# Optimization experiments

Measured on AMD Instinct MI355X. Metric: run time of the kernel, lower is better.

Reference implementation:

```python
import jax, jax.numpy as jnp
import numpy as np

B, N, NPOINT, NSAMPLE = 16, 4096, 1024, 32
RADIUS = 0.2
CHANNELS = [6, 64, 64, 128]
EPS = 1e-5


def farthest_point_sample(xyz, npoint):
    # xyz: [B,N,3] -> idx [B,npoint]; deterministic start at index 0
    b, n, _ = xyz.shape
    def step(carry, _):
        dist, far = carry
        centroid = jnp.take_along_axis(xyz, far[:, None, None], axis=1)  # [B,1,3]
        d = jnp.sum((xyz - centroid) ** 2, axis=-1)  # [B,N]
        dist = jnp.minimum(dist, d)
        return (dist, jnp.argmax(dist, axis=-1).astype(jnp.int32)), far
    init = (jnp.full((b, n), 1e10, dtype=xyz.dtype), jnp.zeros((b,), jnp.int32))
    _, cents = jax.lax.scan(step, init, None, length=npoint)
    return cents.T  # [B,npoint]


def query_ball_point(radius, nsample, xyz, new_xyz):
    # xyz [B,N,3], new_xyz [B,S,3] -> idx [B,S,nsample]
    b, n, _ = xyz.shape
    d2 = (jnp.sum(new_xyz ** 2, -1)[:, :, None]
          + jnp.sum(xyz ** 2, -1)[:, None, :]
          - 2.0 * jnp.einsum('bsc,bnc->bsn', new_xyz, xyz))  # [B,S,N]
    cand = jnp.where(d2 > radius * radius, n, jnp.arange(n, dtype=jnp.int32)[None, None, :])
    # smallest nsample candidate indices (== torch sort[:, :, :nsample])
    neg_top, _ = jax.lax.top_k(-cand, nsample)
    idx = -neg_top  # ascending smallest indices
    first = idx[:, :, 0:1]
    return jnp.where(idx == n, first, idx)


def gather_points(pts, idx):
    # pts [B,N,C], idx [B,S,K] -> [B,S,K,C]
    b, s, k = idx.shape
    flat = idx.reshape(b, s * k)
    out = jnp.take_along_axis(pts, flat[:, :, None], axis=1)
    return out.reshape(b, s, k, pts.shape[-1])


def _forward(xyz, points, params):
    fps_idx = farthest_point_sample(xyz, NPOINT)  # [B,S]
    new_xyz = jnp.take_along_axis(xyz, fps_idx[:, :, None], axis=1)  # [B,S,3]
    idx = query_ball_point(RADIUS, NSAMPLE, xyz, new_xyz)  # [B,S,K]
    grouped_xyz = gather_points(xyz, idx) - new_xyz[:, :, None, :]  # [B,S,K,3]
    grouped_pts = gather_points(points, idx)  # [B,S,K,D]
    x = jnp.concatenate([grouped_xyz, grouped_pts], axis=-1)  # [B,S,K,6]
    for (W, g, bta, m, v) in params:
        x = jnp.einsum('bskc,cd->bskd', x, W)
        x = (x - m) * (g * jax.lax.rsqrt(v + EPS)) + bta  # BN (inference stats)
        x = jax.nn.relu(x)
    feat = jnp.max(x, axis=2)  # [B,S,Cout]
    return new_xyz, feat


def setup_inputs() -> dict:
    key = jax.random.key(0)
    ks = jax.random.split(key, 16)
    xyz = jax.random.uniform(ks[0], (B, N, 3), dtype=jnp.float32)
    points = jax.random.normal(ks[1], (B, N, 3), dtype=jnp.float32)
    inp = {'xyz': xyz, 'points': points}
    ki = 2
    for li in range(3):
        cin, cout = CHANNELS[li], CHANNELS[li + 1]
        inp[f'W{li+1}'] = jax.random.normal(ks[ki], (cin, cout), dtype=jnp.float32) * (1.0 / np.sqrt(cin)); ki += 1
        inp[f'g{li+1}'] = jnp.ones((cout,), jnp.float32)
        inp[f'b{li+1}'] = jnp.zeros((cout,), jnp.float32)
        inp[f'm{li+1}'] = jax.random.normal(ks[ki], (cout,), dtype=jnp.float32) * 0.1; ki += 1
        inp[f'v{li+1}'] = jax.random.uniform(ks[ki], (cout,), dtype=jnp.float32, minval=0.5, maxval=1.5); ki += 1
    return inp


def reference(xyz, points, W1, g1, b1, m1, v1, W2, g2, b2, m2, v2, W3, g3, b3, m3, v3):
    params = [(W1, g1, b1, m1, v1), (W2, g2, b2, m2, v2), (W3, g3, b3, m3, v3)]
    return _forward(xyz, points, params)
```

## Files before the change

### kernel.cpp

```cpp
#include <hip/hip_runtime.h>

#define BATCH   16
#define NPTS    4096
#define NPOINT  1024
#define NSAMPLE 32

typedef float v2f __attribute__((ext_vector_type(2)));
typedef float v4f __attribute__((ext_vector_type(4)));
typedef const __attribute__((address_space(4))) float cs_float;
typedef const __attribute__((address_space(4))) v4f   cs_v4f;

__global__ __attribute__((amdgpu_waves_per_eu(1, 1))) __launch_bounds__(256)
void fps_kernel(const float* __restrict__ xyz, float* __restrict__ new_xyz)
{
#pragma clang fp contract(off)
    const int b    = blockIdx.x;
    const int t    = threadIdx.x;
    const int lane = t & 63;
    const int wv   = t >> 6;
    const float* xb = xyz + (size_t)b * NPTS * 3;

    __shared__ float sxyz4[NPTS * 4];
    __shared__ __align__(16) unsigned long long sCand[2][4];

    v2f px2[8], py2[8], pz2[8], dist2[8];
#pragma unroll
    for (int j = 0; j < 16; ++j) {
        const int n = j * 256 + t;
        float X = xb[n * 3 + 0];
        float Y = xb[n * 3 + 1];
        float Z = xb[n * 3 + 2];
        sxyz4[n * 4 + 0] = X; sxyz4[n * 4 + 1] = Y; sxyz4[n * 4 + 2] = Z;
        asm volatile("" : "+v"(X), "+v"(Y), "+v"(Z));
        const int p = j >> 1;
        if (j & 1) { px2[p].y = X; py2[p].y = Y; pz2[p].y = Z; dist2[p].y = 1e10f; }
        else       { px2[p].x = X; py2[p].x = Y; pz2[p].x = Z; dist2[p].x = 1e10f; }
    }
    __syncthreads();

    float cx = sxyz4[0], cy = sxyz4[1], cz = sxyz4[2];
    float* out = new_xyz + (size_t)b * NPOINT * 3;

    for (int i = 0; i < NPOINT; ++i) {
        if (t == 0) { out[i*3+0] = cx; out[i*3+1] = cy; out[i*3+2] = cz; }

        v2f c2x; c2x.x = cx; c2x.y = cx;
        v2f c2y; c2y.x = cy; c2y.y = cy;
        v2f c2z; c2z.x = cz; c2z.y = cz;
#pragma unroll
        for (int p = 0; p < 8; ++p) {
            v2f dx = px2[p] - c2x;
            v2f dy = py2[p] - c2y;
            v2f dz = pz2[p] - c2z;
            v2f xx = dx * dx;
            v2f yy = dy * dy;
            v2f zz = dz * dz;
            v2f ss = (xx + yy) + zz;
            dist2[p].x = fminf(dist2[p].x, ss.x);
            dist2[p].y = fminf(dist2[p].y, ss.y);
        }

#define D(j) ((j) & 1 ? dist2[(j) >> 1].y : dist2[(j) >> 1].x)
        float mA = fmaxf(fmaxf(D(0),  D(1)),  D(2));
        float mB = fmaxf(fmaxf(D(3),  D(4)),  D(5));
        float mC = fmaxf(fmaxf(D(6),  D(7)),  D(8));
        float mD = fmaxf(fmaxf(D(9),  D(10)), D(11));
        float mE = fmaxf(fmaxf(D(12), D(13)), D(14));
        float mx = fmaxf(fmaxf(fmaxf(mA, mB), mC),
                         fmaxf(fmaxf(mD, mE), D(15)));
        int bj = 15;
#pragma unroll
        for (int j = 15; j >= 0; --j) bj = (D(j) == mx) ? j : bj;
#undef D
        const int bidx = bj * 256 + t;

        unsigned long long cand =
            ((unsigned long long)__float_as_uint(mx) << 32) |
            (unsigned long long)(unsigned int)~bidx;

#define DPP_RED(CTRL, RMASK)                                                   \
        {                                                                      \
            unsigned int oh = (unsigned int)__builtin_amdgcn_update_dpp(       \
                0, (int)(unsigned int)(cand >> 32), (CTRL), (RMASK), 0xF, true);\
            unsigned int ol = (unsigned int)__builtin_amdgcn_update_dpp(       \
                0, (int)(unsigned int)cand, (CTRL), (RMASK), 0xF, true);       \
            unsigned long long o =                                             \
                ((unsigned long long)oh << 32) | (unsigned long long)ol;       \
            if (o > cand) cand = o;                                            \
        }
        DPP_RED(0x121, 0xF)
        DPP_RED(0x122, 0xF)
        DPP_RED(0x124, 0xF)
        DPP_RED(0x128, 0xF)
        DPP_RED(0x142, 0xA)
        DPP_RED(0x143, 0xC)
#undef DPP_RED

        const int par = i & 1;
        if (lane == 63) sCand[par][wv] = cand;
        asm volatile("s_waitcnt lgkmcnt(0)\n\ts_barrier" ::: "memory");

        const ulonglong2* pc = (const ulonglong2*)&sCand[par][0];
        ulonglong2 r0 = pc[0], r1 = pc[1];
        const float4* sx4 = (const float4*)sxyz4;
        float4 f0 = sx4[~(unsigned int)r0.x];
        float4 f1 = sx4[~(unsigned int)r0.y];
        float4 f2 = sx4[~(unsigned int)r1.x];
        float4 f3 = sx4[~(unsigned int)r1.y];
        bool s01 = r0.y > r0.x;
        bool s23 = r1.y > r1.x;
        unsigned long long m01 = s01 ? r0.y : r0.x;
        unsigned long long m23 = s23 ? r1.y : r1.x;
        float4 g01; g01.x = s01 ? f1.x : f0.x; g01.y = s01 ? f1.y : f0.y; g01.z = s01 ? f1.z : f0.z;
        float4 g23; g23.x = s23 ? f3.x : f2.x; g23.y = s23 ? f3.y : f2.y; g23.z = s23 ? f3.z : f2.z;
        bool sF = m23 > m01;
        cx = sF ? g23.x : g01.x;
        cy = sF ? g23.y : g01.y;
        cz = sF ? g23.z : g01.z;
    }
}

__global__ __launch_bounds__(256)
void ball_kernel(const float* __restrict__ xyz, const float* __restrict__ new_xyz,
                 int* __restrict__ idx)
{
    const int q    = blockIdx.x * 4 + (threadIdx.x >> 6);
    const int lane = threadIdx.x & 63;
    const int b    = q >> 10;
    const float* xb = xyz + (size_t)b * NPTS * 3;
    const int NCH = NPTS / 64;

    const float s0 = new_xyz[q*3+0];
    const float s1 = new_xyz[q*3+1];
    const float s2 = new_xyz[q*3+2];
    const float ssum = __fadd_rn(__fadd_rn(__fmul_rn(s0,s0), __fmul_rn(s1,s1)),
                                 __fmul_rn(s2,s2));
    const float r2 = (float)(0.2 * 0.2);

    int* myidx = idx + (size_t)q * NSAMPLE;
    int found = 0;
    int first = -1;

    float x = xb[lane*3+0], y = xb[lane*3+1], z = xb[lane*3+2];
    int c = 0;
    while (true) {
        float xn = 0.f, yn = 0.f, zn = 0.f;
        if (c + 1 < NCH) {
            const float* p = xb + ((size_t)(c + 1) * 64 + lane) * 3;
            xn = p[0]; yn = p[1]; zn = p[2];
        }

        int n = c * 64 + lane;
        float nsum = __fadd_rn(__fadd_rn(__fmul_rn(x,x), __fmul_rn(y,y)), __fmul_rn(z,z));
        float dot  = __fmaf_rn(s2, z, __fmaf_rn(s1, y, __fmul_rn(s0, x)));
        float d2   = __fsub_rn(__fadd_rn(ssum, nsum), __fmul_rn(2.0f, dot));
        bool inb = !(d2 > r2);
        unsigned long long m = __ballot(inb);
        if (first < 0 && m != 0ull) first = c * 64 + (int)__builtin_ctzll(m);
        if (inb) {
            int rank = __popcll(m & ((1ull << lane) - 1ull));
            int slot = found + rank;
            if (slot < NSAMPLE) myidx[slot] = n;
        }
        found += __popcll(m);

        ++c;
        if (c >= NCH || found >= NSAMPLE) break;
        x = xn; y = yn; z = zn;
    }
    if (found > NSAMPLE) found = NSAMPLE;
    for (int slot = found + lane; slot < NSAMPLE; slot += 64) myidx[slot] = first;
}

__global__ __launch_bounds__(256)
void prep_kernel(const float* __restrict__ W1, const float* __restrict__ g1,
                 const float* __restrict__ b1, const float* __restrict__ m1,
                 const float* __restrict__ v1,
                 const float* __restrict__ W2, const float* __restrict__ g2,
                 const float* __restrict__ b2, const float* __restrict__ m2,
                 const float* __restrict__ v2,
                 const float* __restrict__ W3, const float* __restrict__ g3,
                 const float* __restrict__ b3, const float* __restrict__ m3,
                 const float* __restrict__ v3,
                 float* __restrict__ wt)
{
    const int t = threadIdx.x;
    float* Wt1 = wt;
    float* Wt2 = wt + 512;
    float* Wt3 = wt + 512 + 4096;
    float* bi1 = wt + 512 + 4096 + 8192;
    float* bi2 = bi1 + 64;
    float* bi3 = bi2 + 64;

    for (int e = t; e < 64 * 8; e += 256) {
        int d = e >> 3, c = e & 7;
        float sc = g1[d] / sqrtf(v1[d] + 1e-5f);
        Wt1[e] = (c < 6) ? W1[c * 64 + d] * sc : 0.f;
    }
    for (int e = t; e < 64 * 64; e += 256) {
        int d = e >> 6, c = e & 63;
        float sc = g2[d] / sqrtf(v2[d] + 1e-5f);
        Wt2[e] = W2[c * 64 + d] * sc;
    }
    for (int e = t; e < 128 * 64; e += 256) {
        int d = e >> 6, c = e & 63;
        float sc = g3[d] / sqrtf(v3[d] + 1e-5f);
        Wt3[e] = W3[c * 128 + d] * sc;
    }
    for (int d = t; d < 64; d += 256) {
        float s1v = g1[d] / sqrtf(v1[d] + 1e-5f);
        bi1[d] = b1[d] - m1[d] * s1v;
        float s2v = g2[d] / sqrtf(v2[d] + 1e-5f);
        bi2[d] = b2[d] - m2[d] * s2v;
    }
    for (int d = t; d < 128; d += 256) {
        float s3v = g3[d] / sqrtf(v3[d] + 1e-5f);
        bi3[d] = b3[d] - m3[d] * s3v;
    }
}

__global__ __launch_bounds__(256)
void mlp_kernel(const float* __restrict__ xyz, const float* __restrict__ points,
                const float* __restrict__ new_xyz, const int* __restrict__ idx,
                const float* __restrict__ wt,
                float* __restrict__ feat)
{
    const cs_v4f*   Wc1 = (const cs_v4f*)(wt);
    const cs_v4f*   Wc2 = (const cs_v4f*)(wt + 512);
    const cs_v4f*   Wc3 = (const cs_v4f*)(wt + 512 + 4096);
    const cs_float* bi1 = (const cs_float*)(wt + 512 + 4096 + 8192);
    const cs_float* bi2 = bi1 + 64;
    const cs_float* bi3 = bi2 + 64;

    const int tid  = threadIdx.x;
    const int wid  = tid >> 6;
    const int lane = tid & 63;
    const int q = blockIdx.x * 8 + wid * 2 + (lane >> 5);
    const int k = lane & 31;
    const int b = q >> 10;

    const int n = idx[(size_t)q * NSAMPLE + k];
    const float* xp = xyz    + ((size_t)b * NPTS + n) * 3;
    const float* pp = points + ((size_t)b * NPTS + n) * 3;
    const float* nx = new_xyz + (size_t)q * 3;

    const float in0 = __fsub_rn(xp[0], nx[0]);
    const float in1 = __fsub_rn(xp[1], nx[1]);
    const float in2 = __fsub_rn(xp[2], nx[2]);
    const float in3 = pp[0], in4 = pp[1], in5 = pp[2];

    v2f x2[32];
#pragma unroll
    for (int d = 0; d < 64; ++d) {
        v4f wa = Wc1[d * 2 + 0];
        v4f wb = Wc1[d * 2 + 1];
        float acc = bi1[d];
        acc = fmaf(in0, wa.x, acc);
        acc = fmaf(in1, wa.y, acc);
        acc = fmaf(in2, wa.z, acc);
        acc = fmaf(in3, wa.w, acc);
        acc = fmaf(in4, wb.x, acc);
        acc = fmaf(in5, wb.y, acc);
        float r = fmaxf(acc, 0.f);
        if (d & 1) x2[d >> 1].y = r; else x2[d >> 1].x = r;
    }

    v2f y2[32];
#pragma unroll
    for (int d = 0; d < 64; ++d) {
        v2f a2; a2.x = 0.f; a2.y = 0.f;
#pragma unroll
        for (int cc = 0; cc < 16; ++cc) {
            v4f w = Wc2[d * 16 + cc];
            v2f wlo; wlo.x = w.x; wlo.y = w.y;
            v2f whi; whi.x = w.z; whi.y = w.w;
            a2 += x2[2*cc]     * wlo;
            a2 += x2[2*cc + 1] * whi;
        }
        float r = fmaxf(bi2[d] + (a2.x + a2.y), 0.f);
        if (d & 1) y2[d >> 1].y = r; else y2[d >> 1].x = r;
    }

#define POOL_MAX(vv)                                                           \
    {                                                                          \
        float o_;                                                              \
        o_ = __int_as_float(__builtin_amdgcn_update_dpp(                       \
            0, __float_as_int(vv), 0x121, 0xF, 0xF, true));                    \
        vv = fmaxf(vv, o_);                                                    \
        o_ = __int_as_float(__builtin_amdgcn_update_dpp(                       \
            0, __float_as_int(vv), 0x122, 0xF, 0xF, true));                    \
        vv = fmaxf(vv, o_);                                                    \
        o_ = __int_as_float(__builtin_amdgcn_update_dpp(                       \
            0, __float_as_int(vv), 0x124, 0xF, 0xF, true));                    \
        vv = fmaxf(vv, o_);                                                    \
        o_ = __int_as_float(__builtin_amdgcn_update_dpp(                       \
            0, __float_as_int(vv), 0x128, 0xF, 0xF, true));                    \
        vv = fmaxf(vv, o_);                                                    \
        vv = fmaxf(vv, __shfl_xor(vv, 16));                                    \
    }

    float* fq = feat + (size_t)q * 128;
#pragma unroll
    for (int d = 0; d < 128; ++d) {
        v2f a2; a2.x = 0.f; a2.y = 0.f;
#pragma unroll
        for (int cc = 0; cc < 16; ++cc) {
            v4f w = Wc3[d * 16 + cc];
            v2f wlo; wlo.x = w.x; wlo.y = w.y;
            v2f whi; whi.x = w.z; whi.y = w.w;
            a2 += y2[2*cc]     * wlo;
            a2 += y2[2*cc + 1] * whi;
        }
        float vv = fmaxf(bi3[d] + (a2.x + a2.y), 0.f);
        POOL_MAX(vv)
        if (k == 0) fq[d] = vv;
    }
#undef POOL_MAX
}

extern "C" void kernel_launch(void* const* d_in, const int* in_sizes, int n_in,
                              void* d_out, int out_size, void* d_ws, size_t ws_size,
                              hipStream_t stream)
{
    (void)in_sizes; (void)n_in; (void)out_size; (void)ws_size;

    const float* xyz    = (const float*)d_in[0];
    const float* points = (const float*)d_in[1];
    const float* W1 = (const float*)d_in[2];
    const float* g1 = (const float*)d_in[3];
    const float* b1 = (const float*)d_in[4];
    const float* m1 = (const float*)d_in[5];
    const float* v1 = (const float*)d_in[6];
    const float* W2 = (const float*)d_in[7];
    const float* g2 = (const float*)d_in[8];
    const float* b2 = (const float*)d_in[9];
    const float* m2 = (const float*)d_in[10];
    const float* v2 = (const float*)d_in[11];
    const float* W3 = (const float*)d_in[12];
    const float* g3 = (const float*)d_in[13];
    const float* b3 = (const float*)d_in[14];
    const float* m3 = (const float*)d_in[15];
    const float* v3 = (const float*)d_in[16];

    float* out_f    = (float*)d_out;
    float* new_xyz  = out_f;
    float* feat     = out_f + (size_t)BATCH * NPOINT * 3;
    int*   idx      = (int*)d_ws;
    float* wt       = (float*)((char*)d_ws +
                               (size_t)BATCH * NPOINT * NSAMPLE * sizeof(int));

    prep_kernel<<<1, 256, 0, stream>>>(W1, g1, b1, m1, v1,
                                       W2, g2, b2, m2, v2,
                                       W3, g3, b3, m3, v3, wt);
    fps_kernel <<<BATCH, 256, 0, stream>>>(xyz, new_xyz);
    ball_kernel<<<(BATCH * NPOINT) / 4, 256, 0, stream>>>(xyz, new_xyz, idx);
    mlp_kernel <<<(BATCH * NPOINT) / 8, 256, 0, stream>>>(xyz, points, new_xyz, idx,
                                                          wt, feat);
}
```

Baseline: 868.7 us.

## Fuse FPS, ball query and MLP into one persistent kernel with progress flags

Merges the three kernels into one launch. Sixteen blocks run farthest point sampling and publish per-batch progress through release atomics. The remaining blocks spin on those counters and run ball query plus the MLP as soon as centroids appear, so the tail work overlaps the serial FPS instead of waiting for it. Ball query now reads xyz from LDS and writes indices to shared memory, which drops the global idx buffer. The risks are deadlock if consumer blocks fill the device before all FPS blocks are resident, spin-wait overhead, and far fewer consumer blocks (240) doing all the MLP work, which lowers parallelism for that stage.

```diff
diff --git a/kernel.cpp b/kernel.cpp
--- a/kernel.cpp
+++ b/kernel.cpp
@@ -4,173 +4,12 @@
 #define NPTS    4096
 #define NPOINT  1024
 #define NSAMPLE 32
+#define NCB     15
 
 typedef float v2f __attribute__((ext_vector_type(2)));
 typedef float v4f __attribute__((ext_vector_type(4)));
 typedef const __attribute__((address_space(4))) float cs_float;
 typedef const __attribute__((address_space(4))) v4f   cs_v4f;
-
-__global__ __attribute__((amdgpu_waves_per_eu(1, 1))) __launch_bounds__(256)
-void fps_kernel(const float* __restrict__ xyz, float* __restrict__ new_xyz)
-{
-#pragma clang fp contract(off)
-    const int b    = blockIdx.x;
-    const int t    = threadIdx.x;
-    const int lane = t & 63;
-    const int wv   = t >> 6;
-    const float* xb = xyz + (size_t)b * NPTS * 3;
-
-    __shared__ float sxyz4[NPTS * 4];
-    __shared__ __align__(16) unsigned long long sCand[2][4];
-
-    v2f px2[8], py2[8], pz2[8], dist2[8];
-#pragma unroll
-    for (int j = 0; j < 16; ++j) {
-        const int n = j * 256 + t;
-        float X = xb[n * 3 + 0];
-        float Y = xb[n * 3 + 1];
-        float Z = xb[n * 3 + 2];
-        sxyz4[n * 4 + 0] = X; sxyz4[n * 4 + 1] = Y; sxyz4[n * 4 + 2] = Z;
-        asm volatile("" : "+v"(X), "+v"(Y), "+v"(Z));
-        const int p = j >> 1;
-        if (j & 1) { px2[p].y = X; py2[p].y = Y; pz2[p].y = Z; dist2[p].y = 1e10f; }
-        else       { px2[p].x = X; py2[p].x = Y; pz2[p].x = Z; dist2[p].x = 1e10f; }
-    }
-    __syncthreads();
-
-    float cx = sxyz4[0], cy = sxyz4[1], cz = sxyz4[2];
-    float* out = new_xyz + (size_t)b * NPOINT * 3;
-
-    for (int i = 0; i < NPOINT; ++i) {
-        if (t == 0) { out[i*3+0] = cx; out[i*3+1] = cy; out[i*3+2] = cz; }
-
-        v2f c2x; c2x.x = cx; c2x.y = cx;
-        v2f c2y; c2y.x = cy; c2y.y = cy;
-        v2f c2z; c2z.x = cz; c2z.y = cz;
-#pragma unroll
-        for (int p = 0; p < 8; ++p) {
-            v2f dx = px2[p] - c2x;
-            v2f dy = py2[p] - c2y;
-            v2f dz = pz2[p] - c2z;
-            v2f xx = dx * dx;
-            v2f yy = dy * dy;
-            v2f zz = dz * dz;
-            v2f ss = (xx + yy) + zz;
-            dist2[p].x = fminf(dist2[p].x, ss.x);
-            dist2[p].y = fminf(dist2[p].y, ss.y);
-        }
-
-#define D(j) ((j) & 1 ? dist2[(j) >> 1].y : dist2[(j) >> 1].x)
-        float mA = fmaxf(fmaxf(D(0),  D(1)),  D(2));
-        float mB = fmaxf(fmaxf(D(3),  D(4)),  D(5));
-        float mC = fmaxf(fmaxf(D(6),  D(7)),  D(8));
-        float mD = fmaxf(fmaxf(D(9),  D(10)), D(11));
-        float mE = fmaxf(fmaxf(D(12), D(13)), D(14));
-        float mx = fmaxf(fmaxf(fmaxf(mA, mB), mC),
-                         fmaxf(fmaxf(mD, mE), D(15)));
-        int bj = 15;
-#pragma unroll
-        for (int j = 15; j >= 0; --j) bj = (D(j) == mx) ? j : bj;
-#undef D
-        const int bidx = bj * 256 + t;
-
-        unsigned long long cand =
-            ((unsigned long long)__float_as_uint(mx) << 32) |
-            (unsigned long long)(unsigned int)~bidx;
-
-#define DPP_RED(CTRL, RMASK)                                                   \
-        {                                                                      \
-            unsigned int oh = (unsigned int)__builtin_amdgcn_update_dpp(       \
-                0, (int)(unsigned int)(cand >> 32), (CTRL), (RMASK), 0xF, true);\
-            unsigned int ol = (unsigned int)__builtin_amdgcn_update_dpp(       \
-                0, (int)(unsigned int)cand, (CTRL), (RMASK), 0xF, true);       \
-            unsigned long long o =                                             \
-                ((unsigned long long)oh << 32) | (unsigned long long)ol;       \
-            if (o > cand) cand = o;                                            \
-        }
-        DPP_RED(0x121, 0xF)
-        DPP_RED(0x122, 0xF)
-        DPP_RED(0x124, 0xF)
-        DPP_RED(0x128, 0xF)
-        DPP_RED(0x142, 0xA)
-        DPP_RED(0x143, 0xC)
-#undef DPP_RED
-
-        const int par = i & 1;
-        if (lane == 63) sCand[par][wv] = cand;
-        asm volatile("s_waitcnt lgkmcnt(0)\n\ts_barrier" ::: "memory");
-
-        const ulonglong2* pc = (const ulonglong2*)&sCand[par][0];
-        ulonglong2 r0 = pc[0], r1 = pc[1];
-        const float4* sx4 = (const float4*)sxyz4;
-        float4 f0 = sx4[~(unsigned int)r0.x];
-        float4 f1 = sx4[~(unsigned int)r0.y];
-        float4 f2 = sx4[~(unsigned int)r1.x];
-        float4 f3 = sx4[~(unsigned int)r1.y];
-        bool s01 = r0.y > r0.x;
-        bool s23 = r1.y > r1.x;
-        unsigned long long m01 = s01 ? r0.y : r0.x;
-        unsigned long long m23 = s23 ? r1.y : r1.x;
-        float4 g01; g01.x = s01 ? f1.x : f0.x; g01.y = s01 ? f1.y : f0.y; g01.z = s01 ? f1.z : f0.z;
-        float4 g23; g23.x = s23 ? f3.x : f2.x; g23.y = s23 ? f3.y : f2.y; g23.z = s23 ? f3.z : f2.z;
-        bool sF = m23 > m01;
-        cx = sF ? g23.x : g01.x;
-        cy = sF ? g23.y : g01.y;
-        cz = sF ? g23.z : g01.z;
-    }
-}
-
-__global__ __launch_bounds__(256)
-void ball_kernel(const float* __restrict__ xyz, const float* __restrict__ new_xyz,
-                 int* __restrict__ idx)
-{
-    const int q    = blockIdx.x * 4 + (threadIdx.x >> 6);
-    const int lane = threadIdx.x & 63;
-    const int b    = q >> 10;
-    const float* xb = xyz + (size_t)b * NPTS * 3;
-    const int NCH = NPTS / 64;
-
-    const float s0 = new_xyz[q*3+0];
-    const float s1 = new_xyz[q*3+1];
-    const float s2 = new_xyz[q*3+2];
-    const float ssum = __fadd_rn(__fadd_rn(__fmul_rn(s0,s0), __fmul_rn(s1,s1)),
-                                 __fmul_rn(s2,s2));
-    const float r2 = (float)(0.2 * 0.2);
-
-    int* myidx = idx + (size_t)q * NSAMPLE;
-    int found = 0;
-    int first = -1;
-
-    float x = xb[lane*3+0], y = xb[lane*3+1], z = xb[lane*3+2];
-    int c = 0;
-    while (true) {
-        float xn = 0.f, yn = 0.f, zn = 0.f;
-        if (c + 1 < NCH) {
-            const float* p = xb + ((size_t)(c + 1) * 64 + lane) * 3;
-            xn = p[0]; yn = p[1]; zn = p[2];
-        }
-
-        int n = c * 64 + lane;
-        float nsum = __fadd_rn(__fadd_rn(__fmul_rn(x,x), __fmul_rn(y,y)), __fmul_rn(z,z));
-        float dot  = __fmaf_rn(s2, z, __fmaf_rn(s1, y, __fmul_rn(s0, x)));
-        float d2   = __fsub_rn(__fadd_rn(ssum, nsum), __fmul_rn(2.0f, dot));
-        bool inb = !(d2 > r2);
-        unsigned long long m = __ballot(inb);
-        if (first < 0 && m != 0ull) first = c * 64 + (int)__builtin_ctzll(m);
-        if (inb) {
-            int rank = __popcll(m & ((1ull << lane) - 1ull));
-            int slot = found + rank;
-            if (slot < NSAMPLE) myidx[slot] = n;
-        }
-        found += __popcll(m);
-
-        ++c;
-        if (c >= NCH || found >= NSAMPLE) break;
-        x = xn; y = yn; z = zn;
-    }
-    if (found > NSAMPLE) found = NSAMPLE;
-    for (int slot = found + lane; slot < NSAMPLE; slot += 64) myidx[slot] = first;
-}
 
 __global__ __launch_bounds__(256)
 void prep_kernel(const float* __restrict__ W1, const float* __restrict__ g1,
@@ -219,12 +58,138 @@
     }
 }
 
-__global__ __launch_bounds__(256)
-void mlp_kernel(const float* __restrict__ xyz, const float* __restrict__ points,
-                const float* __restrict__ new_xyz, const int* __restrict__ idx,
-                const float* __restrict__ wt,
-                float* __restrict__ feat)
+__global__ __attribute__((amdgpu_waves_per_eu(1, 1))) __launch_bounds__(256)
+void mega_kernel(const float* __restrict__ xyz, const float* __restrict__ points,
+                 const float* __restrict__ wt, int* __restrict__ prog,
+                 float* __restrict__ new_xyz, float* __restrict__ feat)
 {
+    __shared__ __align__(16) float s4[NPTS * 4];
+    __shared__ __align__(16) unsigned long long sC[2][4];
+    __shared__ int sIdxBuf[4][64];
+
+    const int t    = threadIdx.x;
+    const int lane = t & 63;
+    const int wv   = t >> 6;
+
+    if (blockIdx.x < BATCH) {
+#pragma clang fp contract(off)
+        const int b = blockIdx.x;
+        const float* xb = xyz + (size_t)b * NPTS * 3;
+
+        v2f px2[8], py2[8], pz2[8], dist2[8];
+#pragma unroll
+        for (int j = 0; j < 16; ++j) {
+            const int n = j * 256 + t;
+            float X = xb[n * 3 + 0];
+            float Y = xb[n * 3 + 1];
+            float Z = xb[n * 3 + 2];
+            s4[n * 4 + 0] = X; s4[n * 4 + 1] = Y; s4[n * 4 + 2] = Z;
+            asm volatile("" : "+v"(X), "+v"(Y), "+v"(Z));
+            const int p = j >> 1;
+            if (j & 1) { px2[p].y = X; py2[p].y = Y; pz2[p].y = Z; dist2[p].y = 1e10f; }
+            else       { px2[p].x = X; py2[p].x = Y; pz2[p].x = Z; dist2[p].x = 1e10f; }
+        }
+        __syncthreads();
+
+        float cx = s4[0], cy = s4[1], cz = s4[2];
+        float* out = new_xyz + (size_t)b * NPOINT * 3;
+
+        for (int i = 0; i < NPOINT; ++i) {
+            if (t == 0) {
+                out[i*3+0] = cx; out[i*3+1] = cy; out[i*3+2] = cz;
+                __hip_atomic_store(&prog[b], i + 1, __ATOMIC_RELEASE,
+                                   __HIP_MEMORY_SCOPE_AGENT);
+            }
+
+            v2f c2x; c2x.x = cx; c2x.y = cx;
+            v2f c2y; c2y.x = cy; c2y.y = cy;
+            v2f c2z; c2z.x = cz; c2z.y = cz;
+#pragma unroll
+            for (int p = 0; p < 8; ++p) {
+                v2f dx = px2[p] - c2x;
+                v2f dy = py2[p] - c2y;
+                v2f dz = pz2[p] - c2z;
+                v2f xx = dx * dx;
+                v2f yy = dy * dy;
+                v2f zz = dz * dz;
+                v2f ss = (xx + yy) + zz;
+                dist2[p].x = fminf(dist2[p].x, ss.x);
+                dist2[p].y = fminf(dist2[p].y, ss.y);
+            }
+
+#define D(j) ((j) & 1 ? dist2[(j) >> 1].y : dist2[(j) >> 1].x)
+            float mA = fmaxf(fmaxf(D(0),  D(1)),  D(2));
+            float mB = fmaxf(fmaxf(D(3),  D(4)),  D(5));
+            float mC = fmaxf(fmaxf(D(6),  D(7)),  D(8));
+            float mD = fmaxf(fmaxf(D(9),  D(10)), D(11));
+            float mE = fmaxf(fmaxf(D(12), D(13)), D(14));
+            float mx = fmaxf(fmaxf(fmaxf(mA, mB), mC),
+                             fmaxf(fmaxf(mD, mE), D(15)));
+            int bj = 15;
+#pragma unroll
+            for (int j = 15; j >= 0; --j) bj = (D(j) == mx) ? j : bj;
+#undef D
+            const int bidx = bj * 256 + t;
+
+            unsigned long long cand =
+                ((unsigned long long)__float_as_uint(mx) << 32) |
+                (unsigned long long)(unsigned int)~bidx;
+
+#define DPP_RED(CTRL, RMASK)                                                   \
+            {                                                                  \
+                unsigned int oh = (unsigned int)__builtin_amdgcn_update_dpp(   \
+                    0, (int)(unsigned int)(cand >> 32), (CTRL), (RMASK), 0xF, true);\
+                unsigned int ol = (unsigned int)__builtin_amdgcn_update_dpp(   \
+                    0, (int)(unsigned int)cand, (CTRL), (RMASK), 0xF, true);   \
+                unsigned long long o =                                         \
+                    ((unsigned long long)oh << 32) | (unsigned long long)ol;   \
+                if (o > cand) cand = o;                                        \
+            }
+            DPP_RED(0x121, 0xF)
+            DPP_RED(0x122, 0xF)
+            DPP_RED(0x124, 0xF)
+            DPP_RED(0x128, 0xF)
+            DPP_RED(0x142, 0xA)
+            DPP_RED(0x143, 0xC)
+#undef DPP_RED
+
+            const int par = i & 1;
+            if (lane == 63) sC[par][wv] = cand;
+            asm volatile("s_waitcnt lgkmcnt(0)\n\ts_barrier" ::: "memory");
+
+            const ulonglong2* pc = (const ulonglong2*)&sC[par][0];
+            ulonglong2 r0 = pc[0], r1 = pc[1];
+            const float4* sx4 = (const float4*)s4;
+            float4 f0 = sx4[~(unsigned int)r0.x];
+            float4 f1 = sx4[~(unsigned int)r0.y];
+            float4 f2 = sx4[~(unsigned int)r1.x];
+            float4 f3 = sx4[~(unsigned int)r1.y];
+            bool s01 = r0.y > r0.x;
+            bool s23 = r1.y > r1.x;
+            unsigned long long m01 = s01 ? r0.y : r0.x;
+            unsigned long long m23 = s23 ? r1.y : r1.x;
+            float4 g01; g01.x = s01 ? f1.x : f0.x; g01.y = s01 ? f1.y : f0.y; g01.z = s01 ? f1.z : f0.z;
+            float4 g23; g23.x = s23 ? f3.x : f2.x; g23.y = s23 ? f3.y : f2.y; g23.z = s23 ? f3.z : f2.z;
+            bool sF = m23 > m01;
+            cx = sF ? g23.x : g01.x;
+            cy = sF ? g23.y : g01.y;
+            cz = sF ? g23.z : g01.z;
+        }
+        return;
+    }
+
+    const int cb = blockIdx.x - BATCH;
+    const int b  = cb / NCB;
+    const int m  = cb % NCB;
+    const float* xb = xyz + (size_t)b * NPTS * 3;
+
+    for (int e = t; e < NPTS; e += 256) {
+        s4[e * 4 + 0] = xb[e * 3 + 0];
+        s4[e * 4 + 1] = xb[e * 3 + 1];
+        s4[e * 4 + 2] = xb[e * 3 + 2];
+    }
+    __syncthreads();
+
     const cs_v4f*   Wc1 = (const cs_v4f*)(wt);
     const cs_v4f*   Wc2 = (const cs_v4f*)(wt + 512);
     const cs_v4f*   Wc3 = (const cs_v4f*)(wt + 512 + 4096);
@@ -232,90 +197,130 @@
     const cs_float* bi2 = bi1 + 64;
     const cs_float* bi3 = bi2 + 64;
 
-    const int tid  = threadIdx.x;
-    const int wid  = tid >> 6;
-    const int lane = tid & 63;
-    const int q = blockIdx.x * 8 + wid * 2 + (lane >> 5);
-    const int k = lane & 31;
-    const int b = q >> 10;
-
-    const int n = idx[(size_t)q * NSAMPLE + k];
-    const float* xp = xyz    + ((size_t)b * NPTS + n) * 3;
-    const float* pp = points + ((size_t)b * NPTS + n) * 3;
-    const float* nx = new_xyz + (size_t)q * 3;
-
-    const float in0 = __fsub_rn(xp[0], nx[0]);
-    const float in1 = __fsub_rn(xp[1], nx[1]);
-    const float in2 = __fsub_rn(xp[2], nx[2]);
-    const float in3 = pp[0], in4 = pp[1], in5 = pp[2];
-
-    v2f x2[32];
-#pragma unroll
-    for (int d = 0; d < 64; ++d) {
-        v4f wa = Wc1[d * 2 + 0];
-        v4f wb = Wc1[d * 2 + 1];
-        float acc = bi1[d];
-        acc = fmaf(in0, wa.x, acc);
-        acc = fmaf(in1, wa.y, acc);
-        acc = fmaf(in2, wa.z, acc);
-        acc = fmaf(in3, wa.w, acc);
-        acc = fmaf(in4, wb.x, acc);
-        acc = fmaf(in5, wb.y, acc);
-        float r = fmaxf(acc, 0.f);
-        if (d & 1) x2[d >> 1].y = r; else x2[d >> 1].x = r;
-    }
-
-    v2f y2[32];
-#pragma unroll
-    for (int d = 0; d < 64; ++d) {
-        v2f a2; a2.x = 0.f; a2.y = 0.f;
-#pragma unroll
-        for (int cc = 0; cc < 16; ++cc) {
-            v4f w = Wc2[d * 16 + cc];
-            v2f wlo; wlo.x = w.x; wlo.y = w.y;
-            v2f whi; whi.x = w.z; whi.y = w.w;
-            a2 += x2[2*cc]     * wlo;
-            a2 += x2[2*cc + 1] * whi;
-        }
-        float r = fmaxf(bi2[d] + (a2.x + a2.y), 0.f);
-        if (d & 1) y2[d >> 1].y = r; else y2[d >> 1].x = r;
-    }
+    const float r2 = (float)(0.2 * 0.2);
+    const int widx = m * 4 + wv;
+
+    for (int p = widx; p < NPOINT / 2; p += NCB * 4) {
+        const int i1 = 2 * p, i2 = 2 * p + 1;
+
+        while (__hip_atomic_load(&prog[b], __ATOMIC_ACQUIRE,
+                                 __HIP_MEMORY_SCOPE_AGENT) < i2 + 1)
+            __builtin_amdgcn_s_sleep(8);
+
+#pragma unroll
+        for (int sub = 0; sub < 2; ++sub) {
+            const int q = b * NPOINT + (sub ? i2 : i1);
+            const float s0 = new_xyz[q*3+0];
+            const float s1 = new_xyz[q*3+1];
+            const float s2 = new_xyz[q*3+2];
+            const float ssum = __fadd_rn(__fadd_rn(__fmul_rn(s0,s0), __fmul_rn(s1,s1)),
+                                         __fmul_rn(s2,s2));
+            int found = 0;
+            int first = -1;
+            for (int c = 0; c < NPTS / 64 && found < NSAMPLE; ++c) {
+                int n = c * 64 + lane;
+                float x = s4[n*4+0], y = s4[n*4+1], z = s4[n*4+2];
+                float nsum = __fadd_rn(__fadd_rn(__fmul_rn(x,x), __fmul_rn(y,y)),
+                                       __fmul_rn(z,z));
+                float dot  = __fmaf_rn(s2, z, __fmaf_rn(s1, y, __fmul_rn(s0, x)));
+                float d2   = __fsub_rn(__fadd_rn(ssum, nsum), __fmul_rn(2.0f, dot));
+                bool inb = !(d2 > r2);
+                unsigned long long mm = __ballot(inb);
+                if (first < 0 && mm != 0ull) first = c * 64 + (int)__builtin_ctzll(mm);
+                if (inb) {
+                    int rank = __popcll(mm & ((1ull << lane) - 1ull));
+                    int slot = found + rank;
+                    if (slot < NSAMPLE) sIdxBuf[wv][sub * 32 + slot] = n;
+                }
+                found += __popcll(mm);
+            }
+            if (found > NSAMPLE) found = NSAMPLE;
+            for (int slot = found + lane; slot < NSAMPLE; slot += 64)
+                sIdxBuf[wv][sub * 32 + slot] = first;
+        }
+        asm volatile("s_waitcnt lgkmcnt(0)" ::: "memory");
+
+        const int sub = lane >> 5;
+        const int k   = lane & 31;
+        const int qi  = sub ? i2 : i1;
+        const int q   = b * NPOINT + qi;
+        const int n   = sIdxBuf[wv][lane];
+        const float* pp = points + ((size_t)b * NPTS + n) * 3;
+        const float* nx = new_xyz + (size_t)q * 3;
+
+        const float in0 = __fsub_rn(s4[n*4+0], nx[0]);
+        const float in1 = __fsub_rn(s4[n*4+1], nx[1]);
+        const float in2 = __fsub_rn(s4[n*4+2], nx[2]);
+        const float in3 = pp[0], in4 = pp[1], in5 = pp[2];
+
+        v2f x2[32];
+#pragma unroll
+        for (int d = 0; d < 64; ++d) {
+            v4f wa = Wc1[d * 2 + 0];
+            v4f wb = Wc1[d * 2 + 1];
+            float acc = bi1[d];
+            acc = fmaf(in0, wa.x, acc);
+            acc = fmaf(in1, wa.y, acc);
+            acc = fmaf(in2, wa.z, acc);
+            acc = fmaf(in3, wa.w, acc);
+            acc = fmaf(in4, wb.x, acc);
+            acc = fmaf(in5, wb.y, acc);
+            float r = fmaxf(acc, 0.f);
+            if (d & 1) x2[d >> 1].y = r; else x2[d >> 1].x = r;
+        }
+
+        v2f y2[32];
+#pragma unroll
+        for (int d = 0; d < 64; ++d) {
+            v2f a2; a2.x = 0.f; a2.y = 0.f;
+#pragma unroll
+            for (int cc = 0; cc < 16; ++cc) {
+                v4f w = Wc2[d * 16 + cc];
+                v2f wlo; wlo.x = w.x; wlo.y = w.y;
+                v2f whi; whi.x = w.z; whi.y = w.w;
+                a2 += x2[2*cc]     * wlo;
+                a2 += x2[2*cc + 1] * whi;
+            }
+            float r = fmaxf(bi2[d] + (a2.x + a2.y), 0.f);
+            if (d & 1) y2[d >> 1].y = r; else y2[d >> 1].x = r;
+        }
 
 #define POOL_MAX(vv)                                                           \
-    {                                                                          \
-        float o_;                                                              \
-        o_ = __int_as_float(__builtin_amdgcn_update_dpp(                       \
-            0, __float_as_int(vv), 0x121, 0xF, 0xF, true));                    \
-        vv = fmaxf(vv, o_);                                                    \
-        o_ = __int_as_float(__builtin_amdgcn_update_dpp(                       \
-            0, __float_as_int(vv), 0x122, 0xF, 0xF, true));                    \
-        vv = fmaxf(vv, o_);                                                    \
-        o_ = __int_as_float(__builtin_amdgcn_update_dpp(                       \
-            0, __float_as_int(vv), 0x124, 0xF, 0xF, true));                    \
-        vv = fmaxf(vv, o_);                                                    \
-        o_ = __int_as_float(__builtin_amdgcn_update_dpp(                       \
-            0, __float_as_int(vv), 0x128, 0xF, 0xF, true));                    \
-        vv = fmaxf(vv, o_);                                                    \
-        vv = fmaxf(vv, __shfl_xor(vv, 16));                                    \
-    }
-
-    float* fq = feat + (size_t)q * 128;
-#pragma unroll
-    for (int d = 0; d < 128; ++d) {
-        v2f a2; a2.x = 0.f; a2.y = 0.f;
-#pragma unroll
-        for (int cc = 0; cc < 16; ++cc) {
-            v4f w = Wc3[d * 16 + cc];
-            v2f wlo; wlo.x = w.x; wlo.y = w.y;
-            v2f whi; whi.x = w.z; whi.y = w.w;
-            a2 += y2[2*cc]     * wlo;
-            a2 += y2[2*cc + 1] * whi;
-        }
-        float vv = fmaxf(bi3[d] + (a2.x + a2.y), 0.f);
-        POOL_MAX(vv)
-        if (k == 0) fq[d] = vv;
-    }
+        {                                                                      \
+            float o_;                                                          \
+            o_ = __int_as_float(__builtin_amdgcn_update_dpp(                   \
+                0, __float_as_int(vv), 0x121, 0xF, 0xF, true));                \
+            vv = fmaxf(vv, o_);                                                \
+            o_ = __int_as_float(__builtin_amdgcn_update_dpp(                   \
+                0, __float_as_int(vv), 0x122, 0xF, 0xF, true));                \
+            vv = fmaxf(vv, o_);                                                \
+            o_ = __int_as_float(__builtin_amdgcn_update_dpp(                   \
+                0, __float_as_int(vv), 0x124, 0xF, 0xF, true));                \
+            vv = fmaxf(vv, o_);                                                \
+            o_ = __int_as_float(__builtin_amdgcn_update_dpp(                   \
+                0, __float_as_int(vv), 0x128, 0xF, 0xF, true));                \
+            vv = fmaxf(vv, o_);                                                \
+            vv = fmaxf(vv, __shfl_xor(vv, 16));                                \
+        }
+
+        float* fq = feat + (size_t)q * 128;
+#pragma unroll
+        for (int d = 0; d < 128; ++d) {
+            v2f a2; a2.x = 0.f; a2.y = 0.f;
+#pragma unroll
+            for (int cc = 0; cc < 16; ++cc) {
+                v4f w = Wc3[d * 16 + cc];
+                v2f wlo; wlo.x = w.x; wlo.y = w.y;
+                v2f whi; whi.x = w.z; whi.y = w.w;
+                a2 += y2[2*cc]     * wlo;
+                a2 += y2[2*cc + 1] * whi;
+            }
+            float vv = fmaxf(bi3[d] + (a2.x + a2.y), 0.f);
+            POOL_MAX(vv)
+            if (k == 0) fq[d] = vv;
+        }
 #undef POOL_MAX
+    }
 }
 
 extern "C" void kernel_launch(void* const* d_in, const int* in_sizes, int n_in,
@@ -345,15 +350,14 @@
     float* out_f    = (float*)d_out;
     float* new_xyz  = out_f;
     float* feat     = out_f + (size_t)BATCH * NPOINT * 3;
-    int*   idx      = (int*)d_ws;
-    float* wt       = (float*)((char*)d_ws +
-                               (size_t)BATCH * NPOINT * NSAMPLE * sizeof(int));
-
+
+    float* wt   = (float*)((char*)d_ws + 2 * 1024 * 1024);
+    int*   prog = (int*)  ((char*)d_ws + 2 * 1024 * 1024 + 64 * 1024);
+
+    hipMemsetAsync(prog, 0, BATCH * sizeof(int), stream);
     prep_kernel<<<1, 256, 0, stream>>>(W1, g1, b1, m1, v1,
                                        W2, g2, b2, m2, v2,
                                        W3, g3, b3, m3, v3, wt);
-    fps_kernel <<<BATCH, 256, 0, stream>>>(xyz, new_xyz);
-    ball_kernel<<<(BATCH * NPOINT) / 4, 256, 0, stream>>>(xyz, new_xyz, idx);
-    mlp_kernel <<<(BATCH * NPOINT) / 8, 256, 0, stream>>>(xyz, points, new_xyz, idx,
-                                                          wt, feat);
+    mega_kernel<<<BATCH + BATCH * NCB, 256, 0, stream>>>(xyz, points, wt, prog,
+                                                         new_xyz, feat);
 }
```

Measured after the change: 2.937 ms. 238% more time.
